# Kernel tuning notes

Hardware: AMD Instinct MI355X
Metric: run time of the kernel (lower is better)

Reference implementation:

```python
import jax, jax.numpy as jnp
import numpy as np

EPS = 1e-5
NUM_HEADS = 8

def _ln(x, g, b):
    mu = jnp.mean(x, axis=-1, keepdims=True)
    var = jnp.mean(jnp.square(x - mu), axis=-1, keepdims=True)
    return (x - mu) * jax.lax.rsqrt(var + EPS) * g + b

def setup_inputs() -> dict:
    key = jax.random.key(0)
    ks = jax.random.split(key, 20)
    B, S, N, D, F = 16, 12, 325, 256, 2048
    sd = 0.02
    return {
        "x": jax.random.normal(ks[0], (B, S, N, D), jnp.float32),
        "Wq": jax.random.normal(ks[1], (D, D), jnp.float32) * sd,
        "bq": jax.random.normal(ks[2], (D,), jnp.float32) * sd,
        "Wk": jax.random.normal(ks[3], (D, D), jnp.float32) * sd,
        "bk": jax.random.normal(ks[4], (D,), jnp.float32) * sd,
        "Wv": jax.random.normal(ks[5], (D, D), jnp.float32) * sd,
        "bv": jax.random.normal(ks[6], (D,), jnp.float32) * sd,
        "Wo": jax.random.normal(ks[7], (D, D), jnp.float32) * sd,
        "bo": jax.random.normal(ks[8], (D,), jnp.float32) * sd,
        "W1": jax.random.normal(ks[9], (D, F), jnp.float32) * sd,
        "b1": jax.random.normal(ks[10], (F,), jnp.float32) * sd,
        "W2": jax.random.normal(ks[11], (F, D), jnp.float32) * sd,
        "b2": jax.random.normal(ks[12], (D,), jnp.float32) * sd,
        "g1": jax.random.uniform(ks[13], (D,), jnp.float32, 0.5, 1.5),
        "beta1": jax.random.normal(ks[14], (D,), jnp.float32) * sd,
        "g2": jax.random.uniform(ks[15], (D,), jnp.float32, 0.5, 1.5),
        "beta2": jax.random.normal(ks[16], (D,), jnp.float32) * sd,
        "dim": -2,
    }

def reference(x, Wq, bq, Wk, bk, Wv, bv, Wo, bo, W1, b1, W2, b2, g1, beta1, g2, beta2, dim):
    # transpose attention dim to -2 (identity when dim == -2)
    x = jnp.swapaxes(x, dim, -2)
    B, S, N, D = x.shape
    H = NUM_HEADS
    hd = D // H
    residual = x
    # QKV projections
    q = (x @ Wq + bq).reshape(B, S, N, H, hd)
    k = (x @ Wk + bk).reshape(B, S, N, H, hd)
    v = (x @ Wv + bv).reshape(B, S, N, H, hd)
    # attention over node dim (axis -2), per head; scale by sqrt(head_dim)
    scores = jnp.einsum('bsnhd,bsmhd->bshnm', q, k) / jnp.sqrt(jnp.float32(hd))
    attn = jax.nn.softmax(scores, axis=-1)
    out = jnp.einsum('bshnm,bsmhd->bsnhd', attn, v).reshape(B, S, N, D)
    out = out @ Wo + bo
    # dropout is identity (p=0); residual + LN
    out = _ln(residual + out, g1, beta1)
    residual = out
    ff = jax.nn.relu(out @ W1 + b1) @ W2 + b2
    out = _ln(residual + ff, g2, beta2)
    return jnp.swapaxes(out, dim, -2)
```

## Files before the change

### kernel.cpp

```cpp
#include <hip/hip_runtime.h>

typedef unsigned short ushortT;
typedef unsigned short us2 __attribute__((ext_vector_type(2)));
typedef unsigned short us4 __attribute__((ext_vector_type(4)));
typedef short s4 __attribute__((ext_vector_type(4)));
typedef short s8 __attribute__((ext_vector_type(8)));
typedef float f4 __attribute__((ext_vector_type(4)));

__device__ __forceinline__ float bf2f(ushortT u) {
  union { unsigned u; float f; } x; x.u = ((unsigned)u) << 16; return x.f;
}
__device__ __forceinline__ ushortT f2bf(float f) {
  union { float f; unsigned u; } x; x.f = f;
  unsigned r = x.u + 0x7fffu + ((x.u >> 16) & 1u);
  return (ushortT)(r >> 16);
}
__device__ __forceinline__ ushortT bftrunc(float f) {
  union { float f; unsigned u; } x; x.f = f;
  return (ushortT)(x.u >> 16);
}
__device__ __forceinline__ s4 lo4(s8 v) { return __builtin_shufflevector(v, v, 0, 1, 2, 3); }
__device__ __forceinline__ s4 hi4(s8 v) { return __builtin_shufflevector(v, v, 4, 5, 6, 7); }
__device__ __forceinline__ s8 cat(s4 a, s4 b) { return __builtin_shufflevector(a, b, 0, 1, 2, 3, 4, 5, 6, 7); }

__device__ __forceinline__ void gld16(const ushortT* g, ushortT* l) {
  __builtin_amdgcn_global_load_lds(
      (const __attribute__((address_space(1))) void*)g,
      (__attribute__((address_space(3))) void*)l, 16, 0, 0);
}

#define CONV_BLOCKS 15600
__global__ void prep(const float* __restrict__ x,
                     const float* __restrict__ Wq, const float* __restrict__ Wk,
                     const float* __restrict__ Wv, const float* __restrict__ Wo,
                     const float* __restrict__ W1, const float* __restrict__ W2,
                     const float* __restrict__ bq, const float* __restrict__ bk,
                     const float* __restrict__ bv,
                     ushortT* __restrict__ xb, ushortT* __restrict__ WqkvT,
                     ushortT* __restrict__ WoT, ushortT* __restrict__ W1T,
                     ushortT* __restrict__ W2P, float* __restrict__ bqkv)
{
  if (blockIdx.x < CONV_BLOCKS) {
    size_t base = ((size_t)blockIdx.x * 256 + threadIdx.x) * 4;
    f4 v = *(const f4*)(x + base);
    us4 o; o[0]=f2bf(v[0]); o[1]=f2bf(v[1]); o[2]=f2bf(v[2]); o[3]=f2bf(v[3]);
    *(us4*)(xb + base) = o;
    return;
  }
  long e = (long)(blockIdx.x - CONV_BLOCKS) * 256 + threadIdx.x;
  if (e < 196608) {
    int seg = e >> 16; int p = e & 65535; int r = p >> 8, c = p & 255;
    const float* W = seg == 0 ? Wq : (seg == 1 ? Wk : Wv);
    WqkvT[(size_t)(seg * 256 + c) * 256 + r] = f2bf(W[p]);
  } else if (e < 262144) {
    int p = e - 196608; int r = p >> 8, c = p & 255;
    WoT[(size_t)c * 256 + r] = f2bf(Wo[p]);
  } else if (e < 786432) {
    int p = e - 262144; int r = p >> 11, c = p & 2047;
    W1T[(size_t)c * 256 + r] = f2bf(W1[p]);
  } else if (e < 1310720) {
    int p = e - 786432; int r = p >> 8, c = p & 255;
    int rp = (r & ~63) | ((r & 15) << 2) | ((r >> 4) & 3);
    W2P[(size_t)c * 2048 + rp] = f2bf(W2[p]);
  } else {
    int p = (int)(e - 1310720);
    const float* b = (p >> 8) == 0 ? bq : ((p >> 8) == 1 ? bk : bv);
    bqkv[p] = b[p & 255];
  }
}
#define PREP_BLOCKS (CONV_BLOCKS + 5123)

#define BM 128
#define BN 128
#define BK 32

template <typename CT>
__global__ __launch_bounds__(256, 4) void gemm_async(
    const ushortT* __restrict__ A, const ushortT* __restrict__ Bt,
    const float* __restrict__ bias,
    CT* __restrict__ O0, CT* __restrict__ O1, CT* __restrict__ O2,
    int M, int N, int K, int relu, int route, float s0)
{
  __shared__ ushortT As[2][BM * BK];
  __shared__ ushortT Bs[2][BN * BK];
  const int tileN = blockIdx.x * BN;
  const int tileM = blockIdx.y * BM;
  const int tid  = threadIdx.x;
  const int wave = tid >> 6, lane = tid & 63;
  const int wm = (wave >> 1) * 64, wn = (wave & 1) * 64;
  const int lrow = lane & 15;
  const int kq = (lane >> 4) * 8;
  const int crow0 = (lane >> 4) * 4;
  const int ccol  = lane & 15;

  const int srow = wave * 16 + (lane >> 2);
  const int scol = (lane & 3) * 8;
  int ar0 = tileM + srow;        if (ar0 > M - 1) ar0 = M - 1;
  int ar1 = tileM + 64 + srow;   if (ar1 > M - 1) ar1 = M - 1;
  const ushortT* ap0 = A + (size_t)ar0 * K + scol;
  const ushortT* ap1 = A + (size_t)ar1 * K + scol;
  const ushortT* bp0 = Bt + (size_t)(tileN + srow) * K + scol;
  const ushortT* bp1 = Bt + (size_t)(tileN + 64 + srow) * K + scol;
  const int d0 = wave * 512;
  const int d1 = 2048 + wave * 512;

  float bvv[4];
#pragma unroll
  for (int ni = 0; ni < 4; ni++) bvv[ni] = bias[tileN + wn + ni * 16 + ccol];
  asm volatile("" :: "v"(bvv[0]), "v"(bvv[1]), "v"(bvv[2]), "v"(bvv[3]));

  f4 acc[4][4];
#pragma unroll
  for (int i = 0; i < 4; i++)
#pragma unroll
    for (int j = 0; j < 4; j++) acc[i][j] = 0.f;

  gld16(ap0, As[0] + d0); gld16(ap1, As[0] + d1);
  gld16(bp0, Bs[0] + d0); gld16(bp1, Bs[0] + d1);
  ap0 += BK; ap1 += BK; bp0 += BK; bp1 += BK;
  if (BK < K) {
    gld16(ap0, As[1] + d0); gld16(ap1, As[1] + d1);
    gld16(bp0, Bs[1] + d0); gld16(bp1, Bs[1] + d1);
    ap0 += BK; ap1 += BK; bp0 += BK; bp1 += BK;
  }

  int cur = 0;
  for (int k0 = 0; k0 < K; k0 += BK, cur ^= 1) {
    if (k0 + BK < K) asm volatile("s_waitcnt vmcnt(4)" ::: "memory");
    else             asm volatile("s_waitcnt vmcnt(0)" ::: "memory");
    __builtin_amdgcn_s_barrier();
    __builtin_amdgcn_sched_barrier(0);

    s8 af[4], bfr[4];
#pragma unroll
    for (int mi = 0; mi < 4; mi++)
      af[mi] = *(const s8*)(&As[cur][(wm + mi * 16 + lrow) * BK + kq]);
#pragma unroll
    for (int ni = 0; ni < 4; ni++)
      bfr[ni] = *(const s8*)(&Bs[cur][(wn + ni * 16 + lrow) * BK + kq]);
#pragma unroll
    for (int mi = 0; mi < 4; mi++)
#pragma unroll
      for (int ni = 0; ni < 4; ni++)
        acc[mi][ni] = __builtin_amdgcn_mfma_f32_16x16x32_bf16(af[mi], bfr[ni], acc[mi][ni], 0, 0, 0);

    __builtin_amdgcn_s_barrier();
    __builtin_amdgcn_sched_barrier(0);
    if (k0 + 2 * BK < K) {
      gld16(ap0, As[cur] + d0); gld16(ap1, As[cur] + d1);
      gld16(bp0, Bs[cur] + d0); gld16(bp1, Bs[cur] + d1);
      ap0 += BK; ap1 += BK; bp0 += BK; bp1 += BK;
    }
  }

  CT* dst; int col0, ostride;
  float oscale = 1.f;
  if (route) {
    int seg = tileN >> 8;
    dst = seg == 0 ? O0 : (seg == 1 ? O1 : O2);
    col0 = tileN & 255; ostride = 256;
    if (seg == 0) oscale = s0;
  } else {
    dst = O0; col0 = tileN; ostride = N;
  }
#pragma unroll
  for (int mi = 0; mi < 4; mi++) {
#pragma unroll
    for (int ni = 0; ni < 4; ni++) {
      int lcol = wn + ni * 16 + ccol;
#pragma unroll
      for (int r = 0; r < 4; r++) {
        int grow = tileM + wm + mi * 16 + crow0 + r;
        if (grow < M) {
          float v = (acc[mi][ni][r] + bvv[ni]) * oscale;
          if (relu) v = fmaxf(v, 0.f);
          if constexpr (sizeof(CT) == 2)
            dst[(size_t)grow * ostride + col0 + lcol] = f2bf(v);
          else
            dst[(size_t)grow * ostride + col0 + lcol] = v;
        }
      }
    }
  }
}

#define NQ 325
#define NPAD 384
#define KSTR 36
#define VSTR 388
#define PSTR 72

__global__ __launch_bounds__(256, 2) void attn_mfma(
    const ushortT* __restrict__ q, const ushortT* __restrict__ k,
    const ushortT* __restrict__ v, ushortT* __restrict__ out)
{
  __shared__ ushortT ks[NPAD * KSTR];
  __shared__ ushortT vt[32 * VSTR];
  __shared__ ushortT ps[4 * 16 * PSTR];
  const int bs = blockIdx.x >> 3;
  const int h  = blockIdx.x & 7;
  const size_t rowbase = (size_t)bs * NQ;
  const int hcol = h * 32;
  const int tid = threadIdx.x;
  const int wave = tid >> 6, lane = tid & 63;
  const int g = lane >> 4;
  const int c = lane & 15;

  for (int idx = tid; idx < NPAD * 4; idx += 256) {
    int row = idx >> 2, part = idx & 3;
    s8 kv = 0, vv = 0;
    if (row < NQ) {
      kv = *(const s8*)(k + (rowbase + row) * 256 + hcol + part * 8);
      vv = *(const s8*)(v + (rowbase + row) * 256 + hcol + part * 8);
    }
    *(s4*)(ks + row * KSTR + part * 8)     = lo4(kv);
    *(s4*)(ks + row * KSTR + part * 8 + 4) = hi4(kv);
    int pcol = (row & ~63) | ((row & 15) << 2) | ((row >> 4) & 3);
#pragma unroll
    for (int j = 0; j < 8; j++)
      vt[(part * 8 + j) * VSTR + pcol] = (ushortT)vv[j];
  }
  __syncthreads();

  s8 ones;
#pragma unroll
  for (int j = 0; j < 8; j++) ones[j] = (short)0x3F80;

  ushortT* psw = ps + wave * 16 * PSTR;

  for (int strip = wave; strip < 21; strip += 4) {
    const int m0 = strip * 16;
    s8 qf = 0;
    {
      int qrow = m0 + c;
      if (qrow < NQ) qf = *(const s8*)(q + (rowbase + qrow) * 256 + hcol + g * 8);
    }
    f4 ov0 = 0.f, ov1 = 0.f, ovs = 0.f;

    for (int ch = 0; ch < 6; ++ch) {
      const int nbase = ch * 64;
      f4 sc[4];
#pragma unroll
      for (int t = 0; t < 4; ++t) {
        const ushortT* kr = ks + (nbase + t * 16 + c) * KSTR + g * 8;
        s8 kf = cat(*(const s4*)kr, *(const s4*)(kr + 4));
        f4 z = 0.f;
        sc[t] = __builtin_amdgcn_mfma_f32_16x16x32_bf16(qf, kf, z, 0, 0, 0);
      }
#pragma unroll
      for (int t = 0; t < 4; ++t)
#pragma unroll
        for (int r = 0; r < 4; ++r)
          sc[t][r] = __expf(sc[t][r]);
      if (ch == 5) {
#pragma unroll
        for (int t = 0; t < 4; ++t) {
          bool valid = (t == 0) && (c < 5);
#pragma unroll
          for (int r = 0; r < 4; ++r)
            if (!valid) sc[t][r] = 0.f;
        }
      }
#pragma unroll
      for (int r = 0; r < 4; ++r) {
        us4 pw;
#pragma unroll
        for (int t = 0; t < 4; ++t) pw[t] = bftrunc(sc[t][r]);
        *(us4*)(psw + (g * 4 + r) * PSTR + c * 4) = pw;
      }
#pragma unroll
      for (int kt = 0; kt < 2; ++kt) {
        s8 pf = *(const s8*)(psw + c * PSTR + kt * 32 + g * 8);
        ovs = __builtin_amdgcn_mfma_f32_16x16x32_bf16(pf, ones, ovs, 0, 0, 0);
        const ushortT* vr0 = vt + c * VSTR + nbase + kt * 32 + g * 8;
        const ushortT* vr1 = vt + (16 + c) * VSTR + nbase + kt * 32 + g * 8;
        s8 vf0 = cat(*(const s4*)vr0, *(const s4*)(vr0 + 4));
        s8 vf1 = cat(*(const s4*)vr1, *(const s4*)(vr1 + 4));
        ov0 = __builtin_amdgcn_mfma_f32_16x16x32_bf16(pf, vf0, ov0, 0, 0, 0);
        ov1 = __builtin_amdgcn_mfma_f32_16x16x32_bf16(pf, vf1, ov1, 0, 0, 0);
      }
    }
#pragma unroll
    for (int r = 0; r < 4; ++r) {
      int gm = m0 + g * 4 + r;
      if (gm < NQ) {
        float inv = 1.f / ovs[r];
        out[(rowbase + gm) * 256 + hcol + c]      = f2bf(ov0[r] * inv);
        out[(rowbase + gm) * 256 + hcol + 16 + c] = f2bf(ov1[r] * inv);
      }
    }
  }
}

#define HSTR2 72

__global__ __launch_bounds__(512, 2) void ffn_fused(
    const ushortT* __restrict__ y, const ushortT* __restrict__ W1T,
    const float* __restrict__ b1, const ushortT* __restrict__ W2P,
    const float* __restrict__ b2, float* __restrict__ outp, int M)
{
  __shared__ ushortT w1c[2][64 * 256];
  __shared__ ushortT w2c[2][256 * 64];
  __shared__ ushortT hs[128 * HSTR2];
  __shared__ ushortT b1l[2048];

  const int tid = threadIdx.x;
  const int w = tid >> 6, lane = tid & 63;
  const int g = lane >> 4, c = lane & 15;
  const int rq = w >> 1, fh = w & 1;
  const int mq2 = w >> 2, nq = w & 3;
  const int Mtile = blockIdx.x * 128;

  {
    f4 bv = *(const f4*)(b1 + tid * 4);
    us4 o; o[0]=f2bf(bv[0]); o[1]=f2bf(bv[1]); o[2]=f2bf(bv[2]); o[3]=f2bf(bv[3]);
    *(us4*)(b1l + tid * 4) = o;
  }

#pragma unroll
  for (int i = 0; i < 4; ++i) {
    int qq = tid * 8 + i * 4096;
    int r1 = qq >> 8;
    int c1 = (qq & 255) ^ ((r1 & 7) << 3);
    gld16(W1T + (size_t)r1 * 256 + c1, w1c[0] + w * 512 + i * 4096);
    int r2 = qq >> 6;
    int c2 = (qq & 63) ^ ((r2 & 7) << 3);
    gld16(W2P + (size_t)r2 * 2048 + c2, w2c[0] + w * 512 + i * 4096);
  }

  s8 yv[2][8];
#pragma unroll
  for (int mi = 0; mi < 2; ++mi) {
    int yrow = Mtile + rq * 32 + mi * 16 + c; if (yrow > M - 1) yrow = M - 1;
    const ushortT* yp = y + (size_t)yrow * 256 + g * 8;
#pragma unroll
    for (int ksi = 0; ksi < 8; ++ksi) yv[mi][ksi] = *(const s8*)(yp + ksi * 32);
  }

  float b2v[4];
#pragma unroll
  for (int ni = 0; ni < 4; ++ni) b2v[ni] = b2[nq * 64 + ni * 16 + c];

  f4 acc[4][4];
#pragma unroll
  for (int mi = 0; mi < 4; ++mi)
#pragma unroll
    for (int ni = 0; ni < 4; ++ni) acc[mi][ni] = 0.f;

  __syncthreads();

  for (int chn = 0; chn < 32; ++chn) {
    const int b = chn & 1;
    const ushortT* w1b = w1c[b];
    const ushortT* w2b = w2c[b];

    if (chn + 1 < 32) {
      const size_t f1 = (size_t)(chn + 1) * 64 * 256;
      const int k1 = (chn + 1) * 64;
#pragma unroll
      for (int i = 0; i < 4; ++i) {
        int qq = tid * 8 + i * 4096;
        int r1 = qq >> 8;
        int c1 = (qq & 255) ^ ((r1 & 7) << 3);
        gld16(W1T + f1 + (size_t)r1 * 256 + c1, w1c[b ^ 1] + w * 512 + i * 4096);
        int r2 = qq >> 6;
        int c2 = (qq & 63) ^ ((r2 & 7) << 3);
        gld16(W2P + (size_t)r2 * 2048 + k1 + c2, w2c[b ^ 1] + w * 512 + i * 4096);
      }
    }

    f4 sc[2][2];
#pragma unroll
    for (int mi = 0; mi < 2; ++mi)
#pragma unroll
      for (int t = 0; t < 2; ++t) sc[mi][t] = 0.f;
#pragma unroll
    for (int ksi = 0; ksi < 8; ++ksi) {
      int f0 = fh * 32 + c;
      int f1f = fh * 32 + 16 + c;
      s8 wf0 = *(const s8*)(w1b + f0 * 256 + ((ksi * 32 + g * 8) ^ ((c & 7) << 3)));
      s8 wf1 = *(const s8*)(w1b + f1f * 256 + ((ksi * 32 + g * 8) ^ ((c & 7) << 3)));
#pragma unroll
      for (int mi = 0; mi < 2; ++mi) {
        sc[mi][0] = __builtin_amdgcn_mfma_f32_16x16x32_bf16(yv[mi][ksi], wf0, sc[mi][0], 0, 0, 0);
        sc[mi][1] = __builtin_amdgcn_mfma_f32_16x16x32_bf16(yv[mi][ksi], wf1, sc[mi][1], 0, 0, 0);
      }
    }
#pragma unroll
    for (int t = 0; t < 2; ++t) {
      float bv = bf2f(b1l[chn * 64 + fh * 32 + t * 16 + c]);
#pragma unroll
      for (int mi = 0; mi < 2; ++mi)
#pragma unroll
        for (int r = 0; r < 4; ++r) sc[mi][t][r] = fmaxf(sc[mi][t][r] + bv, 0.f);
    }
#pragma unroll
    for (int mi = 0; mi < 2; ++mi)
#pragma unroll
      for (int r = 0; r < 4; ++r) {
        us2 pw; pw[0] = f2bf(sc[mi][0][r]); pw[1] = f2bf(sc[mi][1][r]);
        *(us2*)(hs + (rq * 32 + mi * 16 + g * 4 + r) * HSTR2 + c * 4 + fh * 2) = pw;
      }

    asm volatile("s_waitcnt lgkmcnt(0)" ::: "memory");
    __builtin_amdgcn_s_barrier();
    __builtin_amdgcn_sched_barrier(0);

#pragma unroll
    for (int kt = 0; kt < 2; ++kt) {
      s8 pf[4];
#pragma unroll
      for (int mi = 0; mi < 4; ++mi)
        pf[mi] = *(const s8*)(hs + (mq2 * 64 + mi * 16 + c) * HSTR2 + kt * 32 + g * 8);
#pragma unroll
      for (int ni = 0; ni < 4; ++ni) {
        int n = nq * 64 + ni * 16 + c;
        s8 w2f = *(const s8*)(w2b + n * 64 + ((kt * 32 + g * 8) ^ ((n & 7) << 3)));
#pragma unroll
        for (int mi = 0; mi < 4; ++mi)
          acc[mi][ni] = __builtin_amdgcn_mfma_f32_16x16x32_bf16(pf[mi], w2f, acc[mi][ni], 0, 0, 0);
      }
    }

    asm volatile("s_waitcnt vmcnt(0) lgkmcnt(0)" ::: "memory");
    __builtin_amdgcn_s_barrier();
    __builtin_amdgcn_sched_barrier(0);
  }

#pragma unroll
  for (int mi = 0; mi < 4; ++mi) {
#pragma unroll
    for (int r = 0; r < 4; ++r) {
      int grow = Mtile + mq2 * 64 + mi * 16 + g * 4 + r;
      if (grow < M) {
#pragma unroll
        for (int ni = 0; ni < 4; ++ni)
          outp[(size_t)grow * 256 + nq * 64 + ni * 16 + c] = acc[mi][ni][r] + b2v[ni];
      }
    }
  }
}

template <typename RT, typename VT, typename OT>
__global__ __launch_bounds__(256) void add_ln(
    const RT* __restrict__ res, const VT* __restrict__ val,
    const float* __restrict__ g, const float* __restrict__ beta,
    OT* __restrict__ out, int Mrows)
{
  int row = blockIdx.x * 4 + (threadIdx.x >> 6);
  int lane = threadIdx.x & 63;
  if (row >= Mrows) return;
  float x[4];
  {
    float rvf[4], vvf[4];
    if constexpr (sizeof(RT) == 2) {
      us4 rv = ((const us4*)((const ushortT*)res + (size_t)row * 256))[lane];
      rvf[0]=bf2f(rv[0]); rvf[1]=bf2f(rv[1]); rvf[2]=bf2f(rv[2]); rvf[3]=bf2f(rv[3]);
    } else {
      f4 rv = ((const f4*)((const float*)res + (size_t)row * 256))[lane];
      rvf[0]=rv[0]; rvf[1]=rv[1]; rvf[2]=rv[2]; rvf[3]=rv[3];
    }
    if constexpr (sizeof(VT) == 2) {
      us4 vv = ((const us4*)((const ushortT*)val + (size_t)row * 256))[lane];
      vvf[0]=bf2f(vv[0]); vvf[1]=bf2f(vv[1]); vvf[2]=bf2f(vv[2]); vvf[3]=bf2f(vv[3]);
    } else {
      f4 vv = ((const f4*)((const float*)val + (size_t)row * 256))[lane];
      vvf[0]=vv[0]; vvf[1]=vv[1]; vvf[2]=vv[2]; vvf[3]=vv[3];
    }
#pragma unroll
    for (int j = 0; j < 4; j++) x[j] = rvf[j] + vvf[j];
  }
  float s1 = x[0] + x[1] + x[2] + x[3];
  float s2 = x[0]*x[0] + x[1]*x[1] + x[2]*x[2] + x[3]*x[3];
#pragma unroll
  for (int off = 32; off; off >>= 1) {
    s1 += __shfl_xor(s1, off);
    s2 += __shfl_xor(s2, off);
  }
  float mean = s1 * (1.f / 256.f);
  float var  = s2 * (1.f / 256.f) - mean * mean;
  float rstd = rsqrtf(var + 1e-5f);
  f4 gv = ((const f4*)g)[lane], bv = ((const f4*)beta)[lane];
  if constexpr (sizeof(OT) == 2) {
    us4 o;
#pragma unroll
    for (int j = 0; j < 4; j++)
      o[j] = f2bf((x[j] - mean) * rstd * gv[j] + bv[j]);
    ((us4*)((ushortT*)out + (size_t)row * 256))[lane] = o;
  } else {
    f4 o;
#pragma unroll
    for (int j = 0; j < 4; j++)
      o[j] = (x[j] - mean) * rstd * gv[j] + bv[j];
    ((f4*)((float*)out + (size_t)row * 256))[lane] = o;
  }
}

extern "C" void kernel_launch(void* const* d_in, const int* in_sizes, int n_in,
                              void* d_out, int out_size, void* d_ws, size_t ws_size,
                              hipStream_t stream) {
  const float* x   = (const float*)d_in[0];
  const float* Wq  = (const float*)d_in[1];
  const float* bq  = (const float*)d_in[2];
  const float* Wk  = (const float*)d_in[3];
  const float* bk  = (const float*)d_in[4];
  const float* Wv  = (const float*)d_in[5];
  const float* bv  = (const float*)d_in[6];
  const float* Wo  = (const float*)d_in[7];
  const float* bo  = (const float*)d_in[8];
  const float* W1  = (const float*)d_in[9];
  const float* b1  = (const float*)d_in[10];
  const float* W2  = (const float*)d_in[11];
  const float* b2  = (const float*)d_in[12];
  const float* g1  = (const float*)d_in[13];
  const float* be1 = (const float*)d_in[14];
  const float* g2  = (const float*)d_in[15];
  const float* be2 = (const float*)d_in[16];
  float* outp = (float*)d_out;

  const int M = 16 * 12 * 325;
  const int D = 256;

  ushortT* ws    = (ushortT*)d_ws;
  ushortT* WqkvT = ws;
  ushortT* WoT   = ws + 196608;
  ushortT* W1T   = ws + 262144;
  ushortT* W2P   = ws + 786432;
  float*   bqkv  = (float*)(ws + 1310720);
  ushortT* kb    = ws + 2097152;
  ushortT* vb    = kb + 16777216;
  ushortT* qb = (ushortT*)d_out;
  ushortT* xb = qb + (size_t)M * D;
  ushortT* ob = kb;
  ushortT* y1 = vb;

  dim3 blk(256);

  prep<<<PREP_BLOCKS, blk, 0, stream>>>(x, Wq, Wk, Wv, Wo, W1, W2, bq, bk, bv,
                                        xb, WqkvT, WoT, W1T, W2P, bqkv);

  int mt = (M + BM - 1) / BM;
  const float qscale = 0.17677669529663687f;

  gemm_async<ushortT><<<dim3(768 / BN, mt), blk, 0, stream>>>(
      xb, WqkvT, bqkv, qb, kb, vb, M, 768, D, 0, 1, qscale);

  attn_mfma<<<dim3(192 * 8), blk, 0, stream>>>(qb, kb, vb, qb);

  gemm_async<ushortT><<<dim3(D / BN, mt), blk, 0, stream>>>(
      qb, WoT, bo, ob, ob, ob, M, D, D, 0, 0, 1.f);

  add_ln<float, ushortT, ushortT><<<dim3((M + 3) / 4), blk, 0, stream>>>(x, ob, g1, be1, y1, M);

  ffn_fused<<<dim3((M + 127) / 128), dim3(512), 0, stream>>>(
      y1, W1T, b1, W2P, b2, outp, M);

  add_ln<ushortT, float, float><<<dim3((M + 3) / 4), blk, 0, stream>>>(y1, outp, g2, be2, outp, M);
}
```

Before: 479.9 us.

## Load W2 fragments directly to registers and triple-buffer W1 chunks in LDS

The fused FFN kernel stops staging W2 chunks through shared memory. Each wave now loads its W2 fragments straight from global memory into registers with inline global_load_dwordx4. W1 chunks move to a three-deep LDS ring with prefetch distance two, and vmcnt waits are tuned so the W2 register loads are outstanding while the first GEMM runs. This cuts LDS footprint and LDS read traffic and deepens prefetch, but adds register pressure and relies on precise hand-written vmcnt accounting, which is fragile against compiler reordering.

```diff
diff --git a/kernel.cpp b/kernel.cpp
--- a/kernel.cpp
+++ b/kernel.cpp
@@ -299,8 +299,7 @@
     const float* __restrict__ b1, const ushortT* __restrict__ W2P,
     const float* __restrict__ b2, float* __restrict__ outp, int M)
 {
-  __shared__ ushortT w1c[2][64 * 256];
-  __shared__ ushortT w2c[2][256 * 64];
+  __shared__ ushortT w1c[3][64 * 256];
   __shared__ ushortT hs[128 * HSTR2];
   __shared__ ushortT b1l[2048];
 
@@ -317,17 +316,6 @@
     *(us4*)(b1l + tid * 4) = o;
   }
 
-#pragma unroll
-  for (int i = 0; i < 4; ++i) {
-    int qq = tid * 8 + i * 4096;
-    int r1 = qq >> 8;
-    int c1 = (qq & 255) ^ ((r1 & 7) << 3);
-    gld16(W1T + (size_t)r1 * 256 + c1, w1c[0] + w * 512 + i * 4096);
-    int r2 = qq >> 6;
-    int c2 = (qq & 63) ^ ((r2 & 7) << 3);
-    gld16(W2P + (size_t)r2 * 2048 + c2, w2c[0] + w * 512 + i * 4096);
-  }
-
   s8 yv[2][8];
 #pragma unroll
   for (int mi = 0; mi < 2; ++mi) {
@@ -347,25 +335,45 @@
 #pragma unroll
     for (int ni = 0; ni < 4; ++ni) acc[mi][ni] = 0.f;
 
-  __syncthreads();
+  asm volatile("s_waitcnt vmcnt(0)" ::: "memory");
+
+#pragma unroll
+  for (int ch = 0; ch < 2; ++ch) {
+    const size_t fbase = (size_t)ch * 64 * 256;
+#pragma unroll
+    for (int i = 0; i < 4; ++i) {
+      int qq = tid * 8 + i * 4096;
+      int r1 = qq >> 8;
+      int c1 = (qq & 255) ^ ((r1 & 7) << 3);
+      gld16(W1T + fbase + (size_t)r1 * 256 + c1, w1c[ch] + w * 512 + i * 4096);
+    }
+  }
+  asm volatile("s_waitcnt vmcnt(4) lgkmcnt(0)" ::: "memory");
+  __builtin_amdgcn_s_barrier();
+  __builtin_amdgcn_sched_barrier(0);
 
   for (int chn = 0; chn < 32; ++chn) {
-    const int b = chn & 1;
-    const ushortT* w1b = w1c[b];
-    const ushortT* w2b = w2c[b];
-
-    if (chn + 1 < 32) {
-      const size_t f1 = (size_t)(chn + 1) * 64 * 256;
-      const int k1 = (chn + 1) * 64;
+    const ushortT* w1b = w1c[chn % 3];
+
+    s8 w2f[8];
+#pragma unroll
+    for (int kt = 0; kt < 2; ++kt)
+#pragma unroll
+      for (int ni = 0; ni < 4; ++ni) {
+        const ushortT* p = W2P + (size_t)(nq * 64 + ni * 16 + c) * 2048
+                         + chn * 64 + kt * 32 + g * 8;
+        asm volatile("global_load_dwordx4 %0, %1, off"
+                     : "=v"(w2f[kt * 4 + ni]) : "v"(p) : "memory");
+      }
+    if (chn + 2 < 32) {
+      const size_t fbase = (size_t)(chn + 2) * 64 * 256;
+      ushortT* dst = w1c[(chn + 2) % 3];
 #pragma unroll
       for (int i = 0; i < 4; ++i) {
         int qq = tid * 8 + i * 4096;
         int r1 = qq >> 8;
         int c1 = (qq & 255) ^ ((r1 & 7) << 3);
-        gld16(W1T + f1 + (size_t)r1 * 256 + c1, w1c[b ^ 1] + w * 512 + i * 4096);
-        int r2 = qq >> 6;
-        int c2 = (qq & 63) ^ ((r2 & 7) << 3);
-        gld16(W2P + (size_t)r2 * 2048 + k1 + c2, w2c[b ^ 1] + w * 512 + i * 4096);
+        gld16(W1T + fbase + (size_t)r1 * 256 + c1, dst + w * 512 + i * 4096);
       }
     }
 
@@ -406,6 +414,10 @@
     __builtin_amdgcn_s_barrier();
     __builtin_amdgcn_sched_barrier(0);
 
+    if (chn < 30) asm volatile("s_waitcnt vmcnt(4)" ::: "memory");
+    else          asm volatile("s_waitcnt vmcnt(0)" ::: "memory");
+    __builtin_amdgcn_sched_barrier(0);
+
 #pragma unroll
     for (int kt = 0; kt < 2; ++kt) {
       s8 pf[4];
@@ -413,16 +425,13 @@
       for (int mi = 0; mi < 4; ++mi)
         pf[mi] = *(const s8*)(hs + (mq2 * 64 + mi * 16 + c) * HSTR2 + kt * 32 + g * 8);
 #pragma unroll
-      for (int ni = 0; ni < 4; ++ni) {
-        int n = nq * 64 + ni * 16 + c;
-        s8 w2f = *(const s8*)(w2b + n * 64 + ((kt * 32 + g * 8) ^ ((n & 7) << 3)));
+      for (int ni = 0; ni < 4; ++ni)
 #pragma unroll
         for (int mi = 0; mi < 4; ++mi)
-          acc[mi][ni] = __builtin_amdgcn_mfma_f32_16x16x32_bf16(pf[mi], w2f, acc[mi][ni], 0, 0, 0);
-      }
-    }
-
-    asm volatile("s_waitcnt vmcnt(0) lgkmcnt(0)" ::: "memory");
+          acc[mi][ni] = __builtin_amdgcn_mfma_f32_16x16x32_bf16(pf[mi], w2f[kt * 4 + ni], acc[mi][ni], 0, 0, 0);
+    }
+
+    asm volatile("s_waitcnt lgkmcnt(0)" ::: "memory");
     __builtin_amdgcn_s_barrier();
     __builtin_amdgcn_sched_barrier(0);
   }
```

Result: slower. 550.6 us (+14.7%).

## Halve FFN hidden chunk to 32 to cut LDS and raise occupancy

Applied to the files above, without the earlier changes.

The fused FFN kernel now streams the hidden dimension in 32-wide chunks instead of 64, halving the double-buffered W1/W2 LDS tiles and the hidden-activation staging buffer. The W2 permutation in the prep kernel and the LDS swizzles are changed to match. Launch bounds go from 2 to 4 blocks per multiprocessor to exploit the smaller LDS footprint. The cost is twice as many chunk iterations and barriers, less MFMA work per barrier, and possible register pressure under the tighter launch bound.

```diff
diff --git a/kernel.cpp b/kernel.cpp
--- a/kernel.cpp
+++ b/kernel.cpp
@@ -60,7 +60,7 @@
     W1T[(size_t)c * 256 + r] = f2bf(W1[p]);
   } else if (e < 1310720) {
     int p = e - 786432; int r = p >> 8, c = p & 255;
-    int rp = (r & ~63) | ((r & 15) << 2) | ((r >> 4) & 3);
+    int rp = (r & ~31) | ((r & 15) << 1) | ((r >> 4) & 1);
     W2P[(size_t)c * 2048 + rp] = f2bf(W2[p]);
   } else {
     int p = (int)(e - 1310720);
@@ -292,16 +292,17 @@
   }
 }
 
-#define HSTR2 72
-
-__global__ __launch_bounds__(512, 2) void ffn_fused(
+#define FCH 32
+#define HSTR3 40
+
+__global__ __launch_bounds__(512, 4) void ffn_fused(
     const ushortT* __restrict__ y, const ushortT* __restrict__ W1T,
     const float* __restrict__ b1, const ushortT* __restrict__ W2P,
     const float* __restrict__ b2, float* __restrict__ outp, int M)
 {
-  __shared__ ushortT w1c[2][64 * 256];
-  __shared__ ushortT w2c[2][256 * 64];
-  __shared__ ushortT hs[128 * HSTR2];
+  __shared__ ushortT w1c[2][32 * 256];
+  __shared__ ushortT w2c[2][256 * 32];
+  __shared__ ushortT hs[128 * HSTR3];
   __shared__ ushortT b1l[2048];
 
   const int tid = threadIdx.x;
@@ -318,13 +319,13 @@
   }
 
 #pragma unroll
-  for (int i = 0; i < 4; ++i) {
+  for (int i = 0; i < 2; ++i) {
     int qq = tid * 8 + i * 4096;
     int r1 = qq >> 8;
     int c1 = (qq & 255) ^ ((r1 & 7) << 3);
     gld16(W1T + (size_t)r1 * 256 + c1, w1c[0] + w * 512 + i * 4096);
-    int r2 = qq >> 6;
-    int c2 = (qq & 63) ^ ((r2 & 7) << 3);
+    int r2 = qq >> 5;
+    int c2 = (qq & 31) ^ ((r2 & 3) << 3);
     gld16(W2P + (size_t)r2 * 2048 + c2, w2c[0] + w * 512 + i * 4096);
   }
 
@@ -349,73 +350,62 @@
 
   __syncthreads();
 
-  for (int chn = 0; chn < 32; ++chn) {
+  const int fr = fh * 16 + c;
+
+  for (int chn = 0; chn < 64; ++chn) {
     const int b = chn & 1;
     const ushortT* w1b = w1c[b];
     const ushortT* w2b = w2c[b];
 
-    if (chn + 1 < 32) {
-      const size_t f1 = (size_t)(chn + 1) * 64 * 256;
-      const int k1 = (chn + 1) * 64;
-#pragma unroll
-      for (int i = 0; i < 4; ++i) {
+    if (chn + 1 < 64) {
+      const size_t f1 = (size_t)(chn + 1) * 32 * 256;
+      const int k1 = (chn + 1) * 32;
+#pragma unroll
+      for (int i = 0; i < 2; ++i) {
         int qq = tid * 8 + i * 4096;
         int r1 = qq >> 8;
         int c1 = (qq & 255) ^ ((r1 & 7) << 3);
         gld16(W1T + f1 + (size_t)r1 * 256 + c1, w1c[b ^ 1] + w * 512 + i * 4096);
-        int r2 = qq >> 6;
-        int c2 = (qq & 63) ^ ((r2 & 7) << 3);
+        int r2 = qq >> 5;
+        int c2 = (qq & 31) ^ ((r2 & 3) << 3);
         gld16(W2P + (size_t)r2 * 2048 + k1 + c2, w2c[b ^ 1] + w * 512 + i * 4096);
       }
     }
 
-    f4 sc[2][2];
+    f4 sc[2];
+    sc[0] = 0.f; sc[1] = 0.f;
+#pragma unroll
+    for (int ksi = 0; ksi < 8; ++ksi) {
+      s8 wf = *(const s8*)(w1b + fr * 256 + ((ksi * 32 + g * 8) ^ ((c & 7) << 3)));
+      sc[0] = __builtin_amdgcn_mfma_f32_16x16x32_bf16(yv[0][ksi], wf, sc[0], 0, 0, 0);
+      sc[1] = __builtin_amdgcn_mfma_f32_16x16x32_bf16(yv[1][ksi], wf, sc[1], 0, 0, 0);
+    }
+    {
+      float bv = bf2f(b1l[chn * 32 + fr]);
+#pragma unroll
+      for (int mi = 0; mi < 2; ++mi)
+#pragma unroll
+        for (int r = 0; r < 4; ++r) sc[mi][r] = fmaxf(sc[mi][r] + bv, 0.f);
+    }
 #pragma unroll
     for (int mi = 0; mi < 2; ++mi)
 #pragma unroll
-      for (int t = 0; t < 2; ++t) sc[mi][t] = 0.f;
-#pragma unroll
-    for (int ksi = 0; ksi < 8; ++ksi) {
-      int f0 = fh * 32 + c;
-      int f1f = fh * 32 + 16 + c;
-      s8 wf0 = *(const s8*)(w1b + f0 * 256 + ((ksi * 32 + g * 8) ^ ((c & 7) << 3)));
-      s8 wf1 = *(const s8*)(w1b + f1f * 256 + ((ksi * 32 + g * 8) ^ ((c & 7) << 3)));
-#pragma unroll
-      for (int mi = 0; mi < 2; ++mi) {
-        sc[mi][0] = __builtin_amdgcn_mfma_f32_16x16x32_bf16(yv[mi][ksi], wf0, sc[mi][0], 0, 0, 0);
-        sc[mi][1] = __builtin_amdgcn_mfma_f32_16x16x32_bf16(yv[mi][ksi], wf1, sc[mi][1], 0, 0, 0);
-      }
-    }
-#pragma unroll
-    for (int t = 0; t < 2; ++t) {
-      float bv = bf2f(b1l[chn * 64 + fh * 32 + t * 16 + c]);
-#pragma unroll
-      for (int mi = 0; mi < 2; ++mi)
-#pragma unroll
-        for (int r = 0; r < 4; ++r) sc[mi][t][r] = fmaxf(sc[mi][t][r] + bv, 0.f);
-    }
-#pragma unroll
-    for (int mi = 0; mi < 2; ++mi)
-#pragma unroll
-      for (int r = 0; r < 4; ++r) {
-        us2 pw; pw[0] = f2bf(sc[mi][0][r]); pw[1] = f2bf(sc[mi][1][r]);
-        *(us2*)(hs + (rq * 32 + mi * 16 + g * 4 + r) * HSTR2 + c * 4 + fh * 2) = pw;
-      }
+      for (int r = 0; r < 4; ++r)
+        hs[(rq * 32 + mi * 16 + g * 4 + r) * HSTR3 + c * 2 + fh] = f2bf(sc[mi][r]);
 
     asm volatile("s_waitcnt lgkmcnt(0)" ::: "memory");
     __builtin_amdgcn_s_barrier();
     __builtin_amdgcn_sched_barrier(0);
 
-#pragma unroll
-    for (int kt = 0; kt < 2; ++kt) {
+    {
       s8 pf[4];
 #pragma unroll
       for (int mi = 0; mi < 4; ++mi)
-        pf[mi] = *(const s8*)(hs + (mq2 * 64 + mi * 16 + c) * HSTR2 + kt * 32 + g * 8);
+        pf[mi] = *(const s8*)(hs + (mq2 * 64 + mi * 16 + c) * HSTR3 + g * 8);
 #pragma unroll
       for (int ni = 0; ni < 4; ++ni) {
         int n = nq * 64 + ni * 16 + c;
-        s8 w2f = *(const s8*)(w2b + n * 64 + ((kt * 32 + g * 8) ^ ((n & 7) << 3)));
+        s8 w2f = *(const s8*)(w2b + n * 32 + ((g * 8) ^ ((n & 3) << 3)));
 #pragma unroll
         for (int mi = 0; mi < 4; ++mi)
           acc[mi][ni] = __builtin_amdgcn_mfma_f32_16x16x32_bf16(pf[mi], w2f, acc[mi][ni], 0, 0, 0);
```

New measurement: 751.5 us. 56.6% more time.
